# Performance work log

Measured on AMD Instinct MI355X. Metric: run time of the kernel, lower is better.

The kernel has to match this reference:

```python
import jax, jax.numpy as jnp
import numpy as np

NUM_EMBED = 1024
EMBED_DIM = 256
DECAY = 0.99
EPS = 1e-05
COMMIT = 0.25


def setup_inputs() -> dict:
    key = jax.random.key(0)
    k1, k2, k3 = jax.random.split(key, 3)
    z = jax.random.normal(k1, (64, 32, 32, EMBED_DIM), dtype=jnp.float32)
    lim = 1.0 / NUM_EMBED
    embeddings = jax.random.uniform(k2, (NUM_EMBED, EMBED_DIM), minval=-lim, maxval=lim, dtype=jnp.float32)
    ema_embed = jax.random.uniform(k3, (NUM_EMBED, EMBED_DIM), minval=-lim, maxval=lim, dtype=jnp.float32)
    cluster_size = jnp.zeros((NUM_EMBED,), dtype=jnp.float32)
    return {"z": z, "embeddings": embeddings, "ema_embed": ema_embed, "cluster_size": cluster_size}


def reference(z, embeddings, ema_embed, cluster_size):
    B, H, W, D = z.shape
    zf = z.reshape(-1, D)  # [N, D]
    # squared euclidean distances to codebook: [N, K]
    distances = (zf ** 2).sum(-1, keepdims=True) + (embeddings ** 2).sum(-1) - 2.0 * (zf @ embeddings.T)
    closest = jnp.argmin(distances, axis=-1)  # [N] int
    quantized_indices = closest.reshape(B, H, W)[:, None]  # [B,1,H,W]
    quantized = embeddings[closest].reshape(z.shape)  # gather instead of one-hot GEMM

    # --- training-mode EMA codebook update (buffer math, no grads) ---
    n_i = jnp.zeros((NUM_EMBED,), dtype=zf.dtype).at[closest].add(1.0)  # per-code counts
    new_cluster = cluster_size * DECAY + n_i * (1.0 - DECAY)
    dw = jnp.zeros_like(embeddings).at[closest].add(zf)  # scatter-add of assigned vectors
    new_ema = ema_embed * DECAY + dw * (1.0 - DECAY)
    n = new_cluster.sum()
    new_cluster = (new_cluster + EPS) / (n + NUM_EMBED * EPS) * n
    new_embeddings = new_ema / new_cluster[:, None]

    commitment_loss = jnp.mean((quantized - z) ** 2)
    st_quantized = z + jax.lax.stop_gradient(quantized - z)  # straight-through
    loss = commitment_loss * COMMIT
    return loss, st_quantized, quantized_indices, new_embeddings, new_cluster, new_ema
```

## Files before the change

### kernel.cpp

```cpp
#include <hip/hip_runtime.h>
#include <float.h>
#include <stdint.h>

#define K_EMB 1024
#define D_EMB 256

typedef _Float16 half8 __attribute__((ext_vector_type(8)));
typedef float f32x4_t __attribute__((ext_vector_type(4)));

typedef const __attribute__((address_space(1))) void* as1cv;
typedef __attribute__((address_space(3))) void* as3v;


__global__ void convert_e_kernel(const float* __restrict__ e, _Float16* __restrict__ ehp,
                                 float* __restrict__ t2, unsigned int* __restrict__ flag_cnt) {
  if (blockIdx.x == 0 && threadIdx.x == 0) { flag_cnt[0] = 0; flag_cnt[1] = 0; }
  int row = blockIdx.x * 4 + (threadIdx.x >> 6);
  int lane = threadIdx.x & 63;
  float4 v = ((const float4*)(e + (size_t)row * D_EMB))[lane];
  float s = v.x * v.x + v.y * v.y + v.z * v.z + v.w * v.w;
#pragma unroll
  for (int off = 32; off > 0; off >>= 1) s += __shfl_down(s, off, 64);
  if (lane == 0) t2[row] = s;
  _Float16* dst = ehp + (size_t)row * D_EMB + lane * 4;
  dst[0] = (_Float16)v.x; dst[1] = (_Float16)v.y;
  dst[2] = (_Float16)v.z; dst[3] = (_Float16)v.w;
}


#define BM 128
#define CCH 32
#define NCH (K_EMB / CCH)
#define DELTA 1.5e-4f

__launch_bounds__(256, 3)
__global__ void argmin_mfma_kernel(const float* __restrict__ z,
                                   const _Float16* __restrict__ eh,
                                   const float* __restrict__ t2,
                                   int* __restrict__ closest,
                                   float* __restrict__ idx_out,
                                   unsigned int* __restrict__ flag_cnt,
                                   unsigned int* __restrict__ flag_row,
                                   unsigned int* __restrict__ flag_cand) {
  __shared__ _Float16 ebuf[2][CCH * D_EMB];
  const int tid = threadIdx.x;
  const int wid = tid >> 6;
  const int lane = tid & 63;
  const int c = lane & 15, g = lane >> 4;
  const int row0 = blockIdx.x * BM + wid * 32;

  half8 A[2][8];
#pragma unroll
  for (int fr = 0; fr < 2; ++fr)
#pragma unroll
    for (int df = 0; df < 8; ++df) {
      const float* zp = z + (size_t)(row0 + fr * 16 + c) * D_EMB + df * 32 + g * 8;
      const float4 v0 = *(const float4*)zp;
      const float4 v1 = *(const float4*)(zp + 4);
      half8 h;
      h[0] = (_Float16)v0.x; h[1] = (_Float16)v0.y; h[2] = (_Float16)v0.z; h[3] = (_Float16)v0.w;
      h[4] = (_Float16)v1.x; h[5] = (_Float16)v1.y; h[6] = (_Float16)v1.z; h[7] = (_Float16)v1.w;
      A[fr][df] = h;
    }

  float m1[8], m2[8], m3[8];
  int k1[8], k2[8];
#pragma unroll
  for (int s = 0; s < 8; ++s) { m1[s] = FLT_MAX; m2[s] = FLT_MAX; m3[s] = FLT_MAX; k1[s] = 0; k2[s] = 0; }

#define INS(s, dvv, kkv)                                        \
  {                                                             \
    const float dv_ = (dvv); const int kk_ = (kkv);             \
    const bool lt1 = dv_ < m1[s];                               \
    const bool lt2 = dv_ < m2[s];                               \
    m3[s] = __builtin_amdgcn_fmed3f(m2[s], m3[s], dv_);         \
    const float nm2 = __builtin_amdgcn_fmed3f(m1[s], m2[s], dv_); \
    k2[s] = lt1 ? k1[s] : (lt2 ? kk_ : k2[s]);                  \
    m2[s] = nm2;                                                \
    m1[s] = fminf(m1[s], dv_);                                  \
    k1[s] = lt1 ? kk_ : k1[s];                                  \
  }

  const int rswz = (c & 7) << 3;

  int sgs[4];
#pragma unroll
  for (int u = 0; u < 4; ++u) {
    const int gidx = (wid * 4 + u) * 64 + lane;
    sgs[u] = (gidx & ~7) | ((gidx & 7) ^ ((gidx >> 5) & 7));
  }

#pragma unroll
  for (int u = 0; u < 4; ++u)
    __builtin_amdgcn_global_load_lds((as1cv)(eh + (size_t)sgs[u] * 8),
                                     (as3v)(&ebuf[0][(wid * 4 + u) * 512]), 16, 0, 0);

  int cur = 0;
  for (int cb = 0; cb < NCH; ++cb) {
    __syncthreads();

    if (cb + 1 < NCH) {
      const _Float16* src0 = eh + (size_t)(cb + 1) * (CCH * D_EMB);
#pragma unroll
      for (int u = 0; u < 4; ++u)
        __builtin_amdgcn_global_load_lds((as1cv)(src0 + (size_t)sgs[u] * 8),
                                         (as3v)(&ebuf[cur ^ 1][(wid * 4 + u) * 512]), 16, 0, 0);
    }

    f32x4_t acc[2][2];
#pragma unroll
    for (int fr = 0; fr < 2; ++fr)
#pragma unroll
      for (int fc = 0; fc < 2; ++fc) acc[fr][fc] = (f32x4_t){0.f, 0.f, 0.f, 0.f};

#pragma unroll
    for (int d = 0; d < 8; ++d) {
      half8 Bh[2];
#pragma unroll
      for (int fc = 0; fc < 2; ++fc) {
        const int elem = (d * 32 + g * 8) ^ rswz;
        Bh[fc] = *(const half8*)(&ebuf[cur][(fc * 16 + c) * D_EMB + elem]);
      }
#pragma unroll
      for (int fr = 0; fr < 2; ++fr)
#pragma unroll
        for (int fc = 0; fc < 2; ++fc)
          acc[fr][fc] = __builtin_amdgcn_mfma_f32_16x16x32_f16(A[fr][d], Bh[fc], acc[fr][fc], 0, 0, 0);
    }

#pragma unroll
    for (int fc = 0; fc < 2; ++fc) {
      const int kk = cb * CCH + fc * 16 + c;
      const float t2c = t2[kk];
#pragma unroll
      for (int fr = 0; fr < 2; ++fr)
#pragma unroll
        for (int r = 0; r < 4; ++r) {
          const float dv = fmaf(-2.f, acc[fr][fc][r], t2c);
          const int s = fr * 4 + r;
          INS(s, dv, kk)
        }
    }
    cur ^= 1;
  }

#pragma unroll
  for (int m = 1; m <= 8; m <<= 1) {
#pragma unroll
    for (int s = 0; s < 8; ++s) {
      const float om1 = __shfl_xor(m1[s], m, 64);
      const int ok1 = __shfl_xor(k1[s], m, 64);
      const float om2 = __shfl_xor(m2[s], m, 64);
      const int ok2 = __shfl_xor(k2[s], m, 64);
      const float om3 = __shfl_xor(m3[s], m, 64);
      INS(s, om1, ok1)
      INS(s, om2, ok2)
      m3[s] = fminf(m3[s], om3);
    }
  }
#undef INS

  if (c == 0) {
#pragma unroll
    for (int s = 0; s < 8; ++s) {
      const int fr = s >> 2, r = s & 3;
      const int row = row0 + fr * 16 + g * 4 + r;
      closest[row] = k1[s];
      idx_out[row] = (float)k1[s];
      if (m2[s] - m1[s] < DELTA) {
        const unsigned int p = atomicAdd(flag_cnt, 1u);
        flag_row[p] = (unsigned int)row;
        flag_cand[p] = (unsigned int)k1[s] | ((unsigned int)k2[s] << 10) |
                       ((m3[s] - m1[s] < DELTA) ? (1u << 20) : 0u);
      }
    }
  }
}


__launch_bounds__(256, 4)
__global__ void fixup_pair_kernel(const float* __restrict__ z, const float* __restrict__ emb,
                                  const float* __restrict__ t2,
                                  const unsigned int* __restrict__ flag_cnt,
                                  const unsigned int* __restrict__ flag_row,
                                  const unsigned int* __restrict__ flag_cand,
                                  int* __restrict__ closest, float* __restrict__ idx_out,
                                  unsigned int* __restrict__ flag2_cnt,
                                  unsigned int* __restrict__ flag2) {
  const int tid = threadIdx.x;
  const int q = tid & 3;
  const unsigned int cnt = *flag_cnt;
  const unsigned int nquads = (gridDim.x * 256) >> 2;
  for (unsigned int i = (blockIdx.x * 256 + tid) >> 2; i < cnt; i += nquads) {
    const int row = (int)flag_row[i];
    const unsigned int cand = flag_cand[i];
    if ((cand >> 20) & 1u) {
      if (q == 0) {
        const unsigned int p = atomicAdd(flag2_cnt, 1u);
        flag2[p] = (unsigned int)row;
      }
      continue;
    }
    const int ka = (int)(cand & 1023u), kb = (int)((cand >> 10) & 1023u);
    const float4* zp = (const float4*)(z + (size_t)row * D_EMB) + q * 16;
    const float4* ap = (const float4*)(emb + (size_t)ka * D_EMB) + q * 16;
    const float4* bp = (const float4*)(emb + (size_t)kb * D_EMB) + q * 16;
    float s0 = 0.f, sa = 0.f, sb = 0.f;
#pragma unroll 8
    for (int u = 0; u < 16; ++u) {
      const float4 zv = zp[u], av = ap[u], bv = bp[u];
      s0 = fmaf(zv.x, zv.x, s0); s0 = fmaf(zv.y, zv.y, s0);
      s0 = fmaf(zv.z, zv.z, s0); s0 = fmaf(zv.w, zv.w, s0);
      sa = fmaf(zv.x, av.x, sa); sa = fmaf(zv.y, av.y, sa);
      sa = fmaf(zv.z, av.z, sa); sa = fmaf(zv.w, av.w, sa);
      sb = fmaf(zv.x, bv.x, sb); sb = fmaf(zv.y, bv.y, sb);
      sb = fmaf(zv.z, bv.z, sb); sb = fmaf(zv.w, bv.w, sb);
    }
#pragma unroll
    for (int m = 1; m <= 2; m <<= 1) {
      s0 += __shfl_xor(s0, m, 64);
      sa += __shfl_xor(sa, m, 64);
      sb += __shfl_xor(sb, m, 64);
    }
    if (q == 0) {
      const float da = (s0 + t2[ka]) - 2.f * sa;
      const float db = (s0 + t2[kb]) - 2.f * sb;
      int kbest = ka;
      if (db < da || (db == da && kb < ka)) kbest = kb;
      closest[row] = kbest;
      idx_out[row] = (float)kbest;
    }
  }
}


__launch_bounds__(256, 4)
__global__ void fixup_full_kernel(const float* __restrict__ z, const float* __restrict__ emb,
                                  const float* __restrict__ t2,
                                  const unsigned int* __restrict__ flag2_cnt,
                                  const unsigned int* __restrict__ flag2,
                                  int* __restrict__ closest, float* __restrict__ idx_out) {
  __shared__ float zs[D_EMB];
  __shared__ float t1s;
  __shared__ float redm[4];
  __shared__ int redk[4];
  const int tid = threadIdx.x;
  const int lane = tid & 63, wv = tid >> 6;
  const unsigned int cnt = *flag2_cnt;
  for (unsigned int j = blockIdx.x; j < cnt; j += gridDim.x) {
    __syncthreads();
    const int row = (int)flag2[j];
    if (wv == 0) {
      const float4 v = ((const float4*)(z + (size_t)row * D_EMB))[lane];
      ((float4*)zs)[lane] = v;
      float s = v.x * v.x + v.y * v.y + v.z * v.z + v.w * v.w;
#pragma unroll
      for (int off = 32; off > 0; off >>= 1) s += __shfl_down(s, off, 64);
      if (lane == 0) t1s = s;
    }
    __syncthreads();
    const float4* e0 = (const float4*)(emb + (size_t)(4 * tid + 0) * D_EMB);
    const float4* e1 = (const float4*)(emb + (size_t)(4 * tid + 1) * D_EMB);
    const float4* e2 = (const float4*)(emb + (size_t)(4 * tid + 2) * D_EMB);
    const float4* e3 = (const float4*)(emb + (size_t)(4 * tid + 3) * D_EMB);
    const float4* zp4 = (const float4*)zs;
    float a0 = 0.f, a1 = 0.f, a2 = 0.f, a3 = 0.f;
    for (int i = 0; i < 64; ++i) {
      const float4 z4 = zp4[i];
      const float4 v0 = e0[i], v1 = e1[i], v2 = e2[i], v3 = e3[i];
      a0 = fmaf(z4.x, v0.x, a0); a0 = fmaf(z4.y, v0.y, a0);
      a0 = fmaf(z4.z, v0.z, a0); a0 = fmaf(z4.w, v0.w, a0);
      a1 = fmaf(z4.x, v1.x, a1); a1 = fmaf(z4.y, v1.y, a1);
      a1 = fmaf(z4.z, v1.z, a1); a1 = fmaf(z4.w, v1.w, a1);
      a2 = fmaf(z4.x, v2.x, a2); a2 = fmaf(z4.y, v2.y, a2);
      a2 = fmaf(z4.z, v2.z, a2); a2 = fmaf(z4.w, v2.w, a2);
      a3 = fmaf(z4.x, v3.x, a3); a3 = fmaf(z4.y, v3.y, a3);
      a3 = fmaf(z4.z, v3.z, a3); a3 = fmaf(z4.w, v3.w, a3);
    }
    const float t1v = t1s;
    float best = FLT_MAX;
    int bk = 0x7fffffff;
    const float dvs[4] = {(t1v + t2[4 * tid + 0]) - 2.f * a0,
                          (t1v + t2[4 * tid + 1]) - 2.f * a1,
                          (t1v + t2[4 * tid + 2]) - 2.f * a2,
                          (t1v + t2[4 * tid + 3]) - 2.f * a3};
#pragma unroll
    for (int cc = 0; cc < 4; ++cc) {
      const int k = 4 * tid + cc;
      if (dvs[cc] < best) { best = dvs[cc]; bk = k; }
    }
#pragma unroll
    for (int m = 1; m <= 32; m <<= 1) {
      const float ob = __shfl_xor(best, m, 64);
      const int ok = __shfl_xor(bk, m, 64);
      if (ob < best || (ob == best && ok < bk)) { best = ob; bk = ok; }
    }
    if (lane == 0) { redm[wv] = best; redk[wv] = bk; }
    __syncthreads();
    if (tid == 0) {
      float b = redm[0];
      int k = redk[0];
#pragma unroll
      for (int w = 1; w < 4; ++w)
        if (redm[w] < b || (redm[w] == b && redk[w] < k)) { b = redm[w]; k = redk[w]; }
      closest[row] = k;
      idx_out[row] = (float)k;
    }
  }
}


__global__ void hist1_kernel(const int* __restrict__ closest, unsigned int* __restrict__ rank,
                             unsigned int* __restrict__ blockhist) {
  __shared__ unsigned int lh[K_EMB];
  const int t = threadIdx.x;
  lh[t] = 0;
  __syncthreads();
  const int row = blockIdx.x * 1024 + t;
  rank[row] = atomicAdd(&lh[closest[row]], 1u);
  __syncthreads();
  blockhist[blockIdx.x * K_EMB + t] = lh[t];
}

__global__ void hist2_kernel(unsigned int* __restrict__ blockhist, const float* __restrict__ cs,
                             unsigned int* __restrict__ base, float* __restrict__ newc,
                             float* __restrict__ o_ncl, int nblocks) {
  __shared__ unsigned int sc[K_EMB];
  __shared__ float fr[K_EMB];
  const int bin = threadIdx.x;
  unsigned int s = 0;
  for (int b = 0; b < nblocks; ++b) {
    const unsigned int v = blockhist[b * K_EMB + bin];
    blockhist[b * K_EMB + bin] = s;
    s += v;
  }
  sc[bin] = s;
  __syncthreads();
  for (int off = 1; off < K_EMB; off <<= 1) {
    const unsigned int t = (bin >= off) ? sc[bin - off] : 0u;
    __syncthreads();
    sc[bin] += t;
    __syncthreads();
  }
  base[bin] = sc[bin] - s;
  const float pre = cs[bin] * 0.99f + (float)s * (float)(1.0 - 0.99);
  fr[bin] = pre;
  __syncthreads();
  for (int st = 512; st > 0; st >>= 1) {
    if (bin < st) fr[bin] += fr[bin + st];
    __syncthreads();
  }
  const float n = fr[0];
  const float ncl = (pre + 1e-5f) / (n + (float)(K_EMB * 1e-5)) * n;
  newc[bin] = ncl;
  o_ncl[bin] = ncl;
}

__global__ void hist3_kernel(const int* __restrict__ closest, const unsigned int* __restrict__ rank,
                             const unsigned int* __restrict__ blockhist,
                             const unsigned int* __restrict__ base,
                             unsigned int* __restrict__ sorted) {
  const int t = threadIdx.x;
  const int row = blockIdx.x * 1024 + t;
  const int k = closest[row];
  sorted[base[k] + blockhist[blockIdx.x * K_EMB + k] + rank[row]] = (unsigned int)row;
}


__global__ void dwsum_kernel(const float* __restrict__ z, const unsigned int* __restrict__ sorted,
                             const unsigned int* __restrict__ base, const float* __restrict__ ema,
                             const float* __restrict__ newc, const float* __restrict__ emb,
                             float* __restrict__ o_st, float* __restrict__ o_nema,
                             float* __restrict__ o_nemb, float* __restrict__ loss_part, int N) {
  const int k = blockIdx.x;
  const int lane = threadIdx.x & 63, wv = threadIdx.x >> 6;
  const unsigned int b0 = base[k];
  const unsigned int b1 = (k == K_EMB - 1) ? (unsigned int)N : base[k + 1];
  const float4 ev = ((const float4*)(emb + (size_t)k * D_EMB))[lane];
  float4 acc = {0.f, 0.f, 0.f, 0.f};
  float ls = 0.f;
  for (unsigned int j = b0 + wv; j < b1; j += 4) {
    const unsigned int row = sorted[j];
    const float4 zv = ((const float4*)(z + (size_t)row * D_EMB))[lane];
    const float dx = ev.x - zv.x, dy = ev.y - zv.y, dz = ev.z - zv.z, dww = ev.w - zv.w;
    float* sp = o_st + (size_t)row * D_EMB + lane * 4;
    sp[0] = zv.x + dx; sp[1] = zv.y + dy; sp[2] = zv.z + dz; sp[3] = zv.w + dww;
    ls = fmaf(dx, dx, ls); ls = fmaf(dy, dy, ls);
    ls = fmaf(dz, dz, ls); ls = fmaf(dww, dww, ls);
    acc.x += zv.x; acc.y += zv.y; acc.z += zv.z; acc.w += zv.w;
  }
  __shared__ float4 red[256];
  __shared__ float lred[256];
  red[threadIdx.x] = acc;
  lred[threadIdx.x] = ls;
  __syncthreads();
  for (int s = 128; s > 0; s >>= 1) {
    if (threadIdx.x < s) lred[threadIdx.x] += lred[threadIdx.x + s];
    __syncthreads();
  }
  if (threadIdx.x == 0) loss_part[k] = lred[0];
  if (wv == 0) {
    const float4 a1 = red[64 + lane], a2 = red[128 + lane], a3 = red[192 + lane];
    acc = red[lane];
    acc.x += a1.x + a2.x + a3.x;
    acc.y += a1.y + a2.y + a3.y;
    acc.z += a1.z + a2.z + a3.z;
    acc.w += a1.w + a2.w + a3.w;
    const float4 emv = ((const float4*)ema)[k * 64 + lane];
    const float nc = newc[k];
    const int off = k * D_EMB + lane * 4;
    float ne;
    ne = emv.x * 0.99f + acc.x * (float)(1.0 - 0.99); o_nema[off + 0] = ne; o_nemb[off + 0] = ne / nc;
    ne = emv.y * 0.99f + acc.y * (float)(1.0 - 0.99); o_nema[off + 1] = ne; o_nemb[off + 1] = ne / nc;
    ne = emv.z * 0.99f + acc.z * (float)(1.0 - 0.99); o_nema[off + 2] = ne; o_nemb[off + 2] = ne / nc;
    ne = emv.w * 0.99f + acc.w * (float)(1.0 - 0.99); o_nema[off + 3] = ne; o_nemb[off + 3] = ne / nc;
  }
}

__global__ void loss_final_kernel(const float* __restrict__ loss_part,
                                  float* __restrict__ o_loss, int nrows) {
  const int i = threadIdx.x;
  __shared__ double dred[1024];
  dred[i] = (double)loss_part[i];
  __syncthreads();
  for (int s = 512; s > 0; s >>= 1) {
    if (i < s) dred[i] += dred[i + s];
    __syncthreads();
  }
  if (i == 0) o_loss[0] = (float)(0.25 * (dred[0] / ((double)nrows * (double)D_EMB)));
}


extern "C" void kernel_launch(void* const* d_in, const int* in_sizes, int n_in,
                              void* d_out, int out_size, void* d_ws, size_t ws_size,
                              hipStream_t stream) {
  const float* z = (const float*)d_in[0];
  const float* emb = (const float*)d_in[1];
  const float* ema = (const float*)d_in[2];
  const float* cs = (const float*)d_in[3];
  const int N = in_sizes[0] / D_EMB;
  const int NB = N / 1024;

  float* out = (float*)d_out;
  float* o_loss = out;
  float* o_st = out + 1;
  float* o_idx = o_st + (size_t)N * D_EMB;
  float* o_nemb = o_idx + N;
  float* o_ncl = o_nemb + (size_t)K_EMB * D_EMB;
  float* o_nema = o_ncl + K_EMB;

  float* ws = (float*)d_ws;
  float* t2 = ws;
  float* newc = t2 + K_EMB;
  float* loss_part = newc + K_EMB;
  unsigned int* flag_cnt = (unsigned int*)(loss_part + K_EMB);
  unsigned int* basep = flag_cnt + 4;
  _Float16* ehp = (_Float16*)(basep + K_EMB);
  int* closest = (int*)(ehp + (size_t)K_EMB * D_EMB);
  unsigned int* flag_row = (unsigned int*)(closest + N);
  unsigned int* flag_cand = flag_row + N;
  unsigned int* sorted = flag_cand + N;
  unsigned int* flag2 = sorted + N;

  unsigned int* rank = flag_row;
  unsigned int* blockhist = flag_cand;
  unsigned int* flag2_cnt = flag_cnt + 1;

  convert_e_kernel<<<K_EMB / 4, 256, 0, stream>>>(emb, ehp, t2, flag_cnt);
  argmin_mfma_kernel<<<N / BM, 256, 0, stream>>>(z, ehp, t2, closest, o_idx,
                                                 flag_cnt, flag_row, flag_cand);
  fixup_pair_kernel<<<128, 256, 0, stream>>>(z, emb, t2, flag_cnt, flag_row, flag_cand,
                                             closest, o_idx, flag2_cnt, flag2);
  fixup_full_kernel<<<128, 256, 0, stream>>>(z, emb, t2, flag2_cnt, flag2, closest, o_idx);
  hist1_kernel<<<NB, 1024, 0, stream>>>(closest, rank, blockhist);
  hist2_kernel<<<1, 1024, 0, stream>>>(blockhist, cs, basep, newc, o_ncl, NB);
  hist3_kernel<<<NB, 1024, 0, stream>>>(closest, rank, blockhist, basep, sorted);
  dwsum_kernel<<<K_EMB, 256, 0, stream>>>(z, sorted, basep, ema, newc, emb,
                                          o_st, o_nema, o_nemb, loss_part, N);
  loss_final_kernel<<<1, 1024, 0, stream>>>(loss_part, o_loss, N);
}
```

Measured before the change: 194.1 us.

## Split argmin over codebook halves with a merge kernel and fused fixup

Splits the MFMA distance/argmin kernel across two codebook slices, doubling the grid so more blocks fill the GPU. Each slice writes its top-3 distances and top-2 indices to workspace, and a new merge kernel combines the halves and builds the ambiguity flag lists. The two fixup kernels become one launch, and hist2 now preloads its 64 per-block counts into registers. The cost is an extra launch plus roughly 20 bytes per row per slice of global traffic, and the A tile of z is loaded and converted twice.

```diff
diff --git a/kernel.cpp b/kernel.cpp
--- a/kernel.cpp
+++ b/kernel.cpp
@@ -29,25 +29,28 @@
 
 
 #define BM 128
+#define KSPLIT 2
+#define KSLICE (K_EMB / KSPLIT)
 #define CCH 32
-#define NCH (K_EMB / CCH)
+#define NCHS (KSLICE / CCH)
 #define DELTA 1.5e-4f
 
-__launch_bounds__(256, 3)
+__launch_bounds__(256, 4)
 __global__ void argmin_mfma_kernel(const float* __restrict__ z,
                                    const _Float16* __restrict__ eh,
                                    const float* __restrict__ t2,
-                                   int* __restrict__ closest,
-                                   float* __restrict__ idx_out,
-                                   unsigned int* __restrict__ flag_cnt,
-                                   unsigned int* __restrict__ flag_row,
-                                   unsigned int* __restrict__ flag_cand) {
+                                   float* __restrict__ m1o, unsigned int* __restrict__ k1o,
+                                   float* __restrict__ m2o, unsigned int* __restrict__ k2o,
+                                   float* __restrict__ m3o, int N) {
   __shared__ _Float16 ebuf[2][CCH * D_EMB];
   const int tid = threadIdx.x;
   const int wid = tid >> 6;
   const int lane = tid & 63;
   const int c = lane & 15, g = lane >> 4;
-  const int row0 = blockIdx.x * BM + wid * 32;
+  const int slice = blockIdx.x & (KSPLIT - 1);
+  const int rb = blockIdx.x >> 1;
+  const int row0 = rb * BM + wid * 32;
+  const int kbase = slice * KSLICE;
 
   half8 A[2][8];
 #pragma unroll
@@ -90,17 +93,20 @@
     sgs[u] = (gidx & ~7) | ((gidx & 7) ^ ((gidx >> 5) & 7));
   }
 
-#pragma unroll
-  for (int u = 0; u < 4; ++u)
-    __builtin_amdgcn_global_load_lds((as1cv)(eh + (size_t)sgs[u] * 8),
-                                     (as3v)(&ebuf[0][(wid * 4 + u) * 512]), 16, 0, 0);
+  {
+    const _Float16* src0 = eh + (size_t)kbase * D_EMB;
+#pragma unroll
+    for (int u = 0; u < 4; ++u)
+      __builtin_amdgcn_global_load_lds((as1cv)(src0 + (size_t)sgs[u] * 8),
+                                       (as3v)(&ebuf[0][(wid * 4 + u) * 512]), 16, 0, 0);
+  }
 
   int cur = 0;
-  for (int cb = 0; cb < NCH; ++cb) {
-    __syncthreads();
-
-    if (cb + 1 < NCH) {
-      const _Float16* src0 = eh + (size_t)(cb + 1) * (CCH * D_EMB);
+  for (int cb = 0; cb < NCHS; ++cb) {
+    __syncthreads();
+
+    if (cb + 1 < NCHS) {
+      const _Float16* src0 = eh + (size_t)(kbase + (cb + 1) * CCH) * D_EMB;
 #pragma unroll
       for (int u = 0; u < 4; ++u)
         __builtin_amdgcn_global_load_lds((as1cv)(src0 + (size_t)sgs[u] * 8),
@@ -130,7 +136,7 @@
 
 #pragma unroll
     for (int fc = 0; fc < 2; ++fc) {
-      const int kk = cb * CCH + fc * 16 + c;
+      const int kk = kbase + cb * CCH + fc * 16 + c;
       const float t2c = t2[kk];
 #pragma unroll
       for (int fr = 0; fr < 2; ++fr)
@@ -165,89 +171,109 @@
     for (int s = 0; s < 8; ++s) {
       const int fr = s >> 2, r = s & 3;
       const int row = row0 + fr * 16 + g * 4 + r;
-      closest[row] = k1[s];
-      idx_out[row] = (float)k1[s];
-      if (m2[s] - m1[s] < DELTA) {
-        const unsigned int p = atomicAdd(flag_cnt, 1u);
-        flag_row[p] = (unsigned int)row;
-        flag_cand[p] = (unsigned int)k1[s] | ((unsigned int)k2[s] << 10) |
-                       ((m3[s] - m1[s] < DELTA) ? (1u << 20) : 0u);
+      const size_t idx = (size_t)slice * N + row;
+      m1o[idx] = m1[s]; k1o[idx] = (unsigned int)k1[s];
+      m2o[idx] = m2[s]; k2o[idx] = (unsigned int)k2[s];
+      m3o[idx] = m3[s];
+    }
+  }
+}
+
+
+__global__ void merge_kernel(const float* __restrict__ m1o, const unsigned int* __restrict__ k1o,
+                             const float* __restrict__ m2o, const unsigned int* __restrict__ k2o,
+                             const float* __restrict__ m3o,
+                             int* __restrict__ closest, float* __restrict__ idx_out,
+                             unsigned int* __restrict__ flag_cnt,
+                             unsigned int* __restrict__ flag1_row,
+                             unsigned int* __restrict__ flag1_cand,
+                             unsigned int* __restrict__ flag2, int N) {
+  const int row = blockIdx.x * 256 + threadIdx.x;
+  if (row >= N) return;
+  const float am[3] = {m1o[row], m2o[row], m3o[row]};
+  const int ak[2] = {(int)k1o[row], (int)k2o[row]};
+  const float bm[3] = {m1o[N + row], m2o[N + row], m3o[N + row]};
+  const int bk[2] = {(int)k1o[N + row], (int)k2o[N + row]};
+  float mm[3];
+  int kk[2];
+  int i = 0, j = 0;
+#pragma unroll
+  for (int t = 0; t < 3; ++t) {
+    const bool takeA = (j >= 3) || (i < 3 && am[i] <= bm[j]);
+    const float v = takeA ? am[i] : bm[j];
+    if (t < 2) kk[t] = takeA ? ak[i] : bk[j];
+    mm[t] = v;
+    if (takeA) ++i; else ++j;
+  }
+  closest[row] = kk[0];
+  idx_out[row] = (float)kk[0];
+  if (mm[1] - mm[0] < DELTA) {
+    if (mm[2] - mm[0] < DELTA) {
+      const unsigned int p = atomicAdd(&flag_cnt[1], 1u);
+      flag2[p] = (unsigned int)row;
+    } else {
+      const unsigned int p = atomicAdd(&flag_cnt[0], 1u);
+      flag1_row[p] = (unsigned int)row;
+      flag1_cand[p] = (unsigned int)kk[0] | ((unsigned int)kk[1] << 10);
+    }
+  }
+}
+
+
+__launch_bounds__(256, 4)
+__global__ void fixup_kernel(const float* __restrict__ z, const float* __restrict__ emb,
+                             const float* __restrict__ t2,
+                             const unsigned int* __restrict__ flag_cnt,
+                             const unsigned int* __restrict__ flag1_row,
+                             const unsigned int* __restrict__ flag1_cand,
+                             const unsigned int* __restrict__ flag2,
+                             int* __restrict__ closest, float* __restrict__ idx_out) {
+  const int tid = threadIdx.x;
+  {
+    const int q = tid & 3;
+    const unsigned int cnt = flag_cnt[0];
+    const unsigned int nquads = (gridDim.x * 256) >> 2;
+    for (unsigned int i = (blockIdx.x * 256 + tid) >> 2; i < cnt; i += nquads) {
+      const int row = (int)flag1_row[i];
+      const unsigned int cand = flag1_cand[i];
+      const int ka = (int)(cand & 1023u), kb = (int)((cand >> 10) & 1023u);
+      const float4* zp = (const float4*)(z + (size_t)row * D_EMB) + q * 16;
+      const float4* ap = (const float4*)(emb + (size_t)ka * D_EMB) + q * 16;
+      const float4* bp = (const float4*)(emb + (size_t)kb * D_EMB) + q * 16;
+      float s0 = 0.f, sa = 0.f, sb = 0.f;
+#pragma unroll 8
+      for (int u = 0; u < 16; ++u) {
+        const float4 zv = zp[u], av = ap[u], bv = bp[u];
+        s0 = fmaf(zv.x, zv.x, s0); s0 = fmaf(zv.y, zv.y, s0);
+        s0 = fmaf(zv.z, zv.z, s0); s0 = fmaf(zv.w, zv.w, s0);
+        sa = fmaf(zv.x, av.x, sa); sa = fmaf(zv.y, av.y, sa);
+        sa = fmaf(zv.z, av.z, sa); sa = fmaf(zv.w, av.w, sa);
+        sb = fmaf(zv.x, bv.x, sb); sb = fmaf(zv.y, bv.y, sb);
+        sb = fmaf(zv.z, bv.z, sb); sb = fmaf(zv.w, bv.w, sb);
       }
-    }
-  }
-}
-
-
-__launch_bounds__(256, 4)
-__global__ void fixup_pair_kernel(const float* __restrict__ z, const float* __restrict__ emb,
-                                  const float* __restrict__ t2,
-                                  const unsigned int* __restrict__ flag_cnt,
-                                  const unsigned int* __restrict__ flag_row,
-                                  const unsigned int* __restrict__ flag_cand,
-                                  int* __restrict__ closest, float* __restrict__ idx_out,
-                                  unsigned int* __restrict__ flag2_cnt,
-                                  unsigned int* __restrict__ flag2) {
-  const int tid = threadIdx.x;
-  const int q = tid & 3;
-  const unsigned int cnt = *flag_cnt;
-  const unsigned int nquads = (gridDim.x * 256) >> 2;
-  for (unsigned int i = (blockIdx.x * 256 + tid) >> 2; i < cnt; i += nquads) {
-    const int row = (int)flag_row[i];
-    const unsigned int cand = flag_cand[i];
-    if ((cand >> 20) & 1u) {
+#pragma unroll
+      for (int m = 1; m <= 2; m <<= 1) {
+        s0 += __shfl_xor(s0, m, 64);
+        sa += __shfl_xor(sa, m, 64);
+        sb += __shfl_xor(sb, m, 64);
+      }
       if (q == 0) {
-        const unsigned int p = atomicAdd(flag2_cnt, 1u);
-        flag2[p] = (unsigned int)row;
+        const float da = (s0 + t2[ka]) - 2.f * sa;
+        const float db = (s0 + t2[kb]) - 2.f * sb;
+        int kbest = ka;
+        if (db < da || (db == da && kb < ka)) kbest = kb;
+        closest[row] = kbest;
+        idx_out[row] = (float)kbest;
       }
-      continue;
-    }
-    const int ka = (int)(cand & 1023u), kb = (int)((cand >> 10) & 1023u);
-    const float4* zp = (const float4*)(z + (size_t)row * D_EMB) + q * 16;
-    const float4* ap = (const float4*)(emb + (size_t)ka * D_EMB) + q * 16;
-    const float4* bp = (const float4*)(emb + (size_t)kb * D_EMB) + q * 16;
-    float s0 = 0.f, sa = 0.f, sb = 0.f;
-#pragma unroll 8
-    for (int u = 0; u < 16; ++u) {
-      const float4 zv = zp[u], av = ap[u], bv = bp[u];
-      s0 = fmaf(zv.x, zv.x, s0); s0 = fmaf(zv.y, zv.y, s0);
-      s0 = fmaf(zv.z, zv.z, s0); s0 = fmaf(zv.w, zv.w, s0);
-      sa = fmaf(zv.x, av.x, sa); sa = fmaf(zv.y, av.y, sa);
-      sa = fmaf(zv.z, av.z, sa); sa = fmaf(zv.w, av.w, sa);
-      sb = fmaf(zv.x, bv.x, sb); sb = fmaf(zv.y, bv.y, sb);
-      sb = fmaf(zv.z, bv.z, sb); sb = fmaf(zv.w, bv.w, sb);
-    }
-#pragma unroll
-    for (int m = 1; m <= 2; m <<= 1) {
-      s0 += __shfl_xor(s0, m, 64);
-      sa += __shfl_xor(sa, m, 64);
-      sb += __shfl_xor(sb, m, 64);
-    }
-    if (q == 0) {
-      const float da = (s0 + t2[ka]) - 2.f * sa;
-      const float db = (s0 + t2[kb]) - 2.f * sb;
-      int kbest = ka;
-      if (db < da || (db == da && kb < ka)) kbest = kb;
-      closest[row] = kbest;
-      idx_out[row] = (float)kbest;
-    }
-  }
-}
-
-
-__launch_bounds__(256, 4)
-__global__ void fixup_full_kernel(const float* __restrict__ z, const float* __restrict__ emb,
-                                  const float* __restrict__ t2,
-                                  const unsigned int* __restrict__ flag2_cnt,
-                                  const unsigned int* __restrict__ flag2,
-                                  int* __restrict__ closest, float* __restrict__ idx_out) {
+    }
+  }
   __shared__ float zs[D_EMB];
   __shared__ float t1s;
   __shared__ float redm[4];
   __shared__ int redk[4];
-  const int tid = threadIdx.x;
   const int lane = tid & 63, wv = tid >> 6;
-  const unsigned int cnt = *flag2_cnt;
-  for (unsigned int j = blockIdx.x; j < cnt; j += gridDim.x) {
+  const unsigned int cnt2 = flag_cnt[1];
+  for (unsigned int j = blockIdx.x; j < cnt2; j += gridDim.x) {
     __syncthreads();
     const int row = (int)flag2[j];
     if (wv == 0) {
@@ -329,10 +355,18 @@
   __shared__ float fr[K_EMB];
   const int bin = threadIdx.x;
   unsigned int s = 0;
-  for (int b = 0; b < nblocks; ++b) {
-    const unsigned int v = blockhist[b * K_EMB + bin];
-    blockhist[b * K_EMB + bin] = s;
-    s += v;
+  if (nblocks == 64) {
+    unsigned int v[64];
+#pragma unroll
+    for (int b = 0; b < 64; ++b) v[b] = blockhist[b * K_EMB + bin];
+#pragma unroll
+    for (int b = 0; b < 64; ++b) { const unsigned int t = v[b]; blockhist[b * K_EMB + bin] = s; s += t; }
+  } else {
+    for (int b = 0; b < nblocks; ++b) {
+      const unsigned int v = blockhist[b * K_EMB + bin];
+      blockhist[b * K_EMB + bin] = s;
+      s += v;
+    }
   }
   sc[bin] = s;
   __syncthreads();
@@ -457,21 +491,25 @@
   unsigned int* basep = flag_cnt + 4;
   _Float16* ehp = (_Float16*)(basep + K_EMB);
   int* closest = (int*)(ehp + (size_t)K_EMB * D_EMB);
-  unsigned int* flag_row = (unsigned int*)(closest + N);
-  unsigned int* flag_cand = flag_row + N;
-  unsigned int* sorted = flag_cand + N;
+  unsigned int* flag1_row = (unsigned int*)(closest + N);
+  unsigned int* flag1_cand = flag1_row + N;
+  unsigned int* sorted = flag1_cand + N;
   unsigned int* flag2 = sorted + N;
-
-  unsigned int* rank = flag_row;
-  unsigned int* blockhist = flag_cand;
-  unsigned int* flag2_cnt = flag_cnt + 1;
+  float* m1p = (float*)(flag2 + N);
+  float* m2p = m1p + 2 * (size_t)N;
+  float* m3p = m2p + 2 * (size_t)N;
+  unsigned int* k1p = (unsigned int*)(m3p + 2 * (size_t)N);
+  unsigned int* k2p = k1p + 2 * (size_t)N;
+
+  unsigned int* rank = flag1_row;
+  unsigned int* blockhist = flag1_cand;
 
   convert_e_kernel<<<K_EMB / 4, 256, 0, stream>>>(emb, ehp, t2, flag_cnt);
-  argmin_mfma_kernel<<<N / BM, 256, 0, stream>>>(z, ehp, t2, closest, o_idx,
-                                                 flag_cnt, flag_row, flag_cand);
-  fixup_pair_kernel<<<128, 256, 0, stream>>>(z, emb, t2, flag_cnt, flag_row, flag_cand,
-                                             closest, o_idx, flag2_cnt, flag2);
-  fixup_full_kernel<<<128, 256, 0, stream>>>(z, emb, t2, flag2_cnt, flag2, closest, o_idx);
+  argmin_mfma_kernel<<<(N / BM) * KSPLIT, 256, 0, stream>>>(z, ehp, t2, m1p, k1p, m2p, k2p, m3p, N);
+  merge_kernel<<<N / 256, 256, 0, stream>>>(m1p, k1p, m2p, k2p, m3p, closest, o_idx,
+                                            flag_cnt, flag1_row, flag1_cand, flag2, N);
+  fixup_kernel<<<256, 256, 0, stream>>>(z, emb, t2, flag_cnt, flag1_row, flag1_cand, flag2,
+                                        closest, o_idx);
   hist1_kernel<<<NB, 1024, 0, stream>>>(closest, rank, blockhist);
   hist2_kernel<<<1, 1024, 0, stream>>>(blockhist, cs, basep, newc, o_ncl, NB);
   hist3_kernel<<<NB, 1024, 0, stream>>>(closest, rank, blockhist, basep, sorted);
```

After: 247.8 us. +27.7%, slower.

## Triple-buffer codebook chunks in argmin kernel and batch hist2 prefix loads

Applied to the files above, without the earlier changes.

The argmin MFMA kernel moves from double to triple buffering of fp16 codebook chunks in LDS. Loads are issued two chunks ahead and guarded by a partial vmcnt wait plus a raw s_barrier instead of __syncthreads, so more global-to-LDS latency overlaps compute. Separately, hist2 loads all 64 per-block histogram entries up front before the serial prefix, removing the dependent load chain. The third buffer raises LDS use to 48KB per block, which may lower occupancy against the launch bound of 3.

```diff
diff --git a/kernel.cpp b/kernel.cpp
--- a/kernel.cpp
+++ b/kernel.cpp
@@ -42,7 +42,7 @@
                                    unsigned int* __restrict__ flag_cnt,
                                    unsigned int* __restrict__ flag_row,
                                    unsigned int* __restrict__ flag_cand) {
-  __shared__ _Float16 ebuf[2][CCH * D_EMB];
+  __shared__ _Float16 ebuf[3][CCH * D_EMB];
   const int tid = threadIdx.x;
   const int wid = tid >> 6;
   const int lane = tid & 63;
@@ -90,59 +90,73 @@
     sgs[u] = (gidx & ~7) | ((gidx & 7) ^ ((gidx >> 5) & 7));
   }
 
-#pragma unroll
-  for (int u = 0; u < 4; ++u)
-    __builtin_amdgcn_global_load_lds((as1cv)(eh + (size_t)sgs[u] * 8),
-                                     (as3v)(&ebuf[0][(wid * 4 + u) * 512]), 16, 0, 0);
-
-  int cur = 0;
-  for (int cb = 0; cb < NCH; ++cb) {
-    __syncthreads();
-
-    if (cb + 1 < NCH) {
-      const _Float16* src0 = eh + (size_t)(cb + 1) * (CCH * D_EMB);
-#pragma unroll
-      for (int u = 0; u < 4; ++u)
-        __builtin_amdgcn_global_load_lds((as1cv)(src0 + (size_t)sgs[u] * 8),
-                                         (as3v)(&ebuf[cur ^ 1][(wid * 4 + u) * 512]), 16, 0, 0);
-    }
-
-    f32x4_t acc[2][2];
-#pragma unroll
-    for (int fr = 0; fr < 2; ++fr)
-#pragma unroll
-      for (int fc = 0; fc < 2; ++fc) acc[fr][fc] = (f32x4_t){0.f, 0.f, 0.f, 0.f};
-
-#pragma unroll
-    for (int d = 0; d < 8; ++d) {
-      half8 Bh[2];
-#pragma unroll
-      for (int fc = 0; fc < 2; ++fc) {
-        const int elem = (d * 32 + g * 8) ^ rswz;
-        Bh[fc] = *(const half8*)(&ebuf[cur][(fc * 16 + c) * D_EMB + elem]);
-      }
-#pragma unroll
-      for (int fr = 0; fr < 2; ++fr)
-#pragma unroll
-        for (int fc = 0; fc < 2; ++fc)
-          acc[fr][fc] = __builtin_amdgcn_mfma_f32_16x16x32_f16(A[fr][d], Bh[fc], acc[fr][fc], 0, 0, 0);
-    }
-
-#pragma unroll
-    for (int fc = 0; fc < 2; ++fc) {
-      const int kk = cb * CCH + fc * 16 + c;
-      const float t2c = t2[kk];
-#pragma unroll
-      for (int fr = 0; fr < 2; ++fr)
-#pragma unroll
-        for (int r = 0; r < 4; ++r) {
-          const float dv = fmaf(-2.f, acc[fr][fc][r], t2c);
-          const int s = fr * 4 + r;
-          INS(s, dv, kk)
-        }
-    }
-    cur ^= 1;
-  }
+#define ISSUE(cbn, buf)                                                              \
+  {                                                                                  \
+    const _Float16* src_ = eh + (size_t)(cbn) * (CCH * D_EMB);                       \
+    _Float16* db_ = &ebuf[buf][0];                                                   \
+    _Pragma("unroll")                                                                \
+    for (int u = 0; u < 4; ++u)                                                      \
+      __builtin_amdgcn_global_load_lds((as1cv)(src_ + (size_t)sgs[u] * 8),           \
+                                       (as3v)(db_ + (wid * 4 + u) * 512), 16, 0, 0); \
+  }
+
+#define COMPUTE(rb_, cb_)                                                            \
+  {                                                                                  \
+    f32x4_t acc[2][2];                                                               \
+    _Pragma("unroll")                                                                \
+    for (int fr = 0; fr < 2; ++fr)                                                   \
+      _Pragma("unroll")                                                              \
+      for (int fc = 0; fc < 2; ++fc) acc[fr][fc] = (f32x4_t){0.f, 0.f, 0.f, 0.f};    \
+    _Pragma("unroll")                                                                \
+    for (int d = 0; d < 8; ++d) {                                                    \
+      half8 Bh[2];                                                                   \
+      _Pragma("unroll")                                                              \
+      for (int fc = 0; fc < 2; ++fc) {                                               \
+        const int elem = (d * 32 + g * 8) ^ rswz;                                    \
+        Bh[fc] = *(const half8*)(&ebuf[rb_][(fc * 16 + c) * D_EMB + elem]);          \
+      }                                                                              \
+      _Pragma("unroll")                                                              \
+      for (int fr = 0; fr < 2; ++fr)                                                 \
+        _Pragma("unroll")                                                            \
+        for (int fc = 0; fc < 2; ++fc)                                               \
+          acc[fr][fc] = __builtin_amdgcn_mfma_f32_16x16x32_f16(A[fr][d], Bh[fc],     \
+                                                               acc[fr][fc], 0, 0, 0);\
+    }                                                                                \
+    _Pragma("unroll")                                                                \
+    for (int fc = 0; fc < 2; ++fc) {                                                 \
+      const int kk = (cb_)*CCH + fc * 16 + c;                                        \
+      const float t2c = t2[kk];                                                      \
+      _Pragma("unroll")                                                              \
+      for (int fr = 0; fr < 2; ++fr)                                                 \
+        _Pragma("unroll")                                                            \
+        for (int r = 0; r < 4; ++r) {                                                \
+          const float dv = fmaf(-2.f, acc[fr][fc][r], t2c);                          \
+          const int s = fr * 4 + r;                                                  \
+          INS(s, dv, kk)                                                             \
+        }                                                                            \
+    }                                                                                \
+  }
+
+  ISSUE(0, 0)
+  ISSUE(1, 1)
+
+  for (int cb = 0; cb < NCH - 1; ++cb) {
+    asm volatile("s_waitcnt vmcnt(4)" ::: "memory");
+    __builtin_amdgcn_s_barrier();
+    __builtin_amdgcn_sched_barrier(0);
+    if (cb + 2 < NCH) ISSUE(cb + 2, (cb + 2) % 3)
+    const int rb = cb % 3;
+    COMPUTE(rb, cb)
+  }
+  asm volatile("s_waitcnt vmcnt(0)" ::: "memory");
+  __builtin_amdgcn_s_barrier();
+  __builtin_amdgcn_sched_barrier(0);
+  {
+    const int rb = (NCH - 1) % 3;
+    COMPUTE(rb, NCH - 1)
+  }
+#undef COMPUTE
+#undef ISSUE
 
 #pragma unroll
   for (int m = 1; m <= 8; m <<= 1) {
@@ -329,10 +343,18 @@
   __shared__ float fr[K_EMB];
   const int bin = threadIdx.x;
   unsigned int s = 0;
-  for (int b = 0; b < nblocks; ++b) {
-    const unsigned int v = blockhist[b * K_EMB + bin];
-    blockhist[b * K_EMB + bin] = s;
-    s += v;
+  if (nblocks == 64) {
+    unsigned int v[64];
+#pragma unroll
+    for (int b = 0; b < 64; ++b) v[b] = blockhist[b * K_EMB + bin];
+#pragma unroll
+    for (int b = 0; b < 64; ++b) { const unsigned int t = v[b]; blockhist[b * K_EMB + bin] = s; s += t; }
+  } else {
+    for (int b = 0; b < nblocks; ++b) {
+      const unsigned int v = blockhist[b * K_EMB + bin];
+      blockhist[b * K_EMB + bin] = s;
+      s += v;
+    }
   }
   sc[bin] = s;
   __syncthreads();
```

Measured after the change: 187.8 us. 3.3% less time.

## Stream codebook directly into registers per wave, drop LDS staging

Applied to the files above, without the earlier changes.

The argmin kernel moves from 256-thread blocks that stage codebook chunks through double-buffered LDS with async global-to-LDS loads to single-wave blocks of 32 rows. Each wave loads its 16-code B fragments straight from global memory into registers, double-buffered by hand. This removes LDS traffic and block-wide barriers, but each wave now reads the whole fp16 codebook itself and relies on L2 for reuse. Separately, the histogram prefix pass unrolls its per-block loads into a register array when there are 64 blocks, so the reads can be in flight together.

```diff
diff --git a/kernel.cpp b/kernel.cpp
--- a/kernel.cpp
+++ b/kernel.cpp
@@ -7,9 +7,6 @@
 
 typedef _Float16 half8 __attribute__((ext_vector_type(8)));
 typedef float f32x4_t __attribute__((ext_vector_type(4)));
-
-typedef const __attribute__((address_space(1))) void* as1cv;
-typedef __attribute__((address_space(3))) void* as3v;
 
 
 __global__ void convert_e_kernel(const float* __restrict__ e, _Float16* __restrict__ ehp,
@@ -28,12 +25,9 @@
 }
 
 
-#define BM 128
-#define CCH 32
-#define NCH (K_EMB / CCH)
 #define DELTA 1.5e-4f
 
-__launch_bounds__(256, 3)
+__launch_bounds__(64, 2)
 __global__ void argmin_mfma_kernel(const float* __restrict__ z,
                                    const _Float16* __restrict__ eh,
                                    const float* __restrict__ t2,
@@ -42,12 +36,9 @@
                                    unsigned int* __restrict__ flag_cnt,
                                    unsigned int* __restrict__ flag_row,
                                    unsigned int* __restrict__ flag_cand) {
-  __shared__ _Float16 ebuf[2][CCH * D_EMB];
-  const int tid = threadIdx.x;
-  const int wid = tid >> 6;
-  const int lane = tid & 63;
+  const int lane = threadIdx.x;
   const int c = lane & 15, g = lane >> 4;
-  const int row0 = blockIdx.x * BM + wid * 32;
+  const int row0 = blockIdx.x * 32;
 
   half8 A[2][8];
 #pragma unroll
@@ -81,68 +72,43 @@
     k1[s] = lt1 ? kk_ : k1[s];                                  \
   }
 
-  const int rswz = (c & 7) << 3;
-
-  int sgs[4];
-#pragma unroll
-  for (int u = 0; u < 4; ++u) {
-    const int gidx = (wid * 4 + u) * 64 + lane;
-    sgs[u] = (gidx & ~7) | ((gidx & 7) ^ ((gidx >> 5) & 7));
-  }
-
-#pragma unroll
-  for (int u = 0; u < 4; ++u)
-    __builtin_amdgcn_global_load_lds((as1cv)(eh + (size_t)sgs[u] * 8),
-                                     (as3v)(&ebuf[0][(wid * 4 + u) * 512]), 16, 0, 0);
-
-  int cur = 0;
-  for (int cb = 0; cb < NCH; ++cb) {
-    __syncthreads();
-
-    if (cb + 1 < NCH) {
-      const _Float16* src0 = eh + (size_t)(cb + 1) * (CCH * D_EMB);
-#pragma unroll
-      for (int u = 0; u < 4; ++u)
-        __builtin_amdgcn_global_load_lds((as1cv)(src0 + (size_t)sgs[u] * 8),
-                                         (as3v)(&ebuf[cur ^ 1][(wid * 4 + u) * 512]), 16, 0, 0);
-    }
-
-    f32x4_t acc[2][2];
-#pragma unroll
-    for (int fr = 0; fr < 2; ++fr)
-#pragma unroll
-      for (int fc = 0; fc < 2; ++fc) acc[fr][fc] = (f32x4_t){0.f, 0.f, 0.f, 0.f};
-
-#pragma unroll
-    for (int d = 0; d < 8; ++d) {
-      half8 Bh[2];
-#pragma unroll
-      for (int fc = 0; fc < 2; ++fc) {
-        const int elem = (d * 32 + g * 8) ^ rswz;
-        Bh[fc] = *(const half8*)(&ebuf[cur][(fc * 16 + c) * D_EMB + elem]);
-      }
-#pragma unroll
-      for (int fr = 0; fr < 2; ++fr)
-#pragma unroll
-        for (int fc = 0; fc < 2; ++fc)
-          acc[fr][fc] = __builtin_amdgcn_mfma_f32_16x16x32_f16(A[fr][d], Bh[fc], acc[fr][fc], 0, 0, 0);
-    }
-
-#pragma unroll
-    for (int fc = 0; fc < 2; ++fc) {
-      const int kk = cb * CCH + fc * 16 + c;
-      const float t2c = t2[kk];
-#pragma unroll
-      for (int fr = 0; fr < 2; ++fr)
-#pragma unroll
-        for (int r = 0; r < 4; ++r) {
-          const float dv = fmaf(-2.f, acc[fr][fc][r], t2c);
-          const int s = fr * 4 + r;
-          INS(s, dv, kk)
-        }
-    }
-    cur ^= 1;
-  }
+  const _Float16* bbase = eh + (size_t)c * D_EMB + g * 8;
+
+#define LOADB(buf, kt)                                                         \
+  _Pragma("unroll")                                                            \
+  for (int d = 0; d < 8; ++d)                                                  \
+    buf[d] = *(const half8*)(bbase + (size_t)(kt) * (16 * D_EMB) + d * 32);
+
+#define COMPUTE_TILE(buf, kt)                                                  \
+  {                                                                            \
+    f32x4_t acc0 = (f32x4_t){0.f, 0.f, 0.f, 0.f};                              \
+    f32x4_t acc1 = (f32x4_t){0.f, 0.f, 0.f, 0.f};                              \
+    _Pragma("unroll")                                                          \
+    for (int d = 0; d < 8; ++d) {                                              \
+      acc0 = __builtin_amdgcn_mfma_f32_16x16x32_f16(A[0][d], buf[d], acc0, 0, 0, 0); \
+      acc1 = __builtin_amdgcn_mfma_f32_16x16x32_f16(A[1][d], buf[d], acc1, 0, 0, 0); \
+    }                                                                          \
+    const int kk = (kt)*16 + c;                                                \
+    const float t2c = t2[kk];                                                  \
+    _Pragma("unroll")                                                          \
+    for (int r = 0; r < 4; ++r) {                                              \
+      const float dv0 = fmaf(-2.f, acc0[r], t2c);                              \
+      INS(r, dv0, kk)                                                          \
+      const float dv1 = fmaf(-2.f, acc1[r], t2c);                              \
+      INS(4 + r, dv1, kk)                                                      \
+    }                                                                          \
+  }
+
+  half8 B0[8], B1[8];
+  LOADB(B0, 0)
+  for (int kt = 0; kt < 64; kt += 2) {
+    LOADB(B1, kt + 1)
+    COMPUTE_TILE(B0, kt)
+    if (kt + 2 < 64) LOADB(B0, kt + 2)
+    COMPUTE_TILE(B1, kt + 1)
+  }
+#undef COMPUTE_TILE
+#undef LOADB
 
 #pragma unroll
   for (int m = 1; m <= 8; m <<= 1) {
@@ -329,10 +295,18 @@
   __shared__ float fr[K_EMB];
   const int bin = threadIdx.x;
   unsigned int s = 0;
-  for (int b = 0; b < nblocks; ++b) {
-    const unsigned int v = blockhist[b * K_EMB + bin];
-    blockhist[b * K_EMB + bin] = s;
-    s += v;
+  if (nblocks == 64) {
+    unsigned int v[64];
+#pragma unroll
+    for (int b = 0; b < 64; ++b) v[b] = blockhist[b * K_EMB + bin];
+#pragma unroll
+    for (int b = 0; b < 64; ++b) { const unsigned int t = v[b]; blockhist[b * K_EMB + bin] = s; s += t; }
+  } else {
+    for (int b = 0; b < nblocks; ++b) {
+      const unsigned int v = blockhist[b * K_EMB + bin];
+      blockhist[b * K_EMB + bin] = s;
+      s += v;
+    }
   }
   sc[bin] = s;
   __syncthreads();
@@ -467,8 +441,8 @@
   unsigned int* flag2_cnt = flag_cnt + 1;
 
   convert_e_kernel<<<K_EMB / 4, 256, 0, stream>>>(emb, ehp, t2, flag_cnt);
-  argmin_mfma_kernel<<<N / BM, 256, 0, stream>>>(z, ehp, t2, closest, o_idx,
-                                                 flag_cnt, flag_row, flag_cand);
+  argmin_mfma_kernel<<<N / 32, 64, 0, stream>>>(z, ehp, t2, closest, o_idx,
+                                                flag_cnt, flag_row, flag_cand);
   fixup_pair_kernel<<<128, 256, 0, stream>>>(z, emb, t2, flag_cnt, flag_row, flag_cand,
                                              closest, o_idx, flag2_cnt, flag2);
   fixup_full_kernel<<<128, 256, 0, stream>>>(z, emb, t2, flag2_cnt, flag2, closest, o_idx);
```

Result: slower. 267.8 us (+38.0%).
